# Kernel tuning notes

Hardware: AMD Instinct MI355X
Metric: run time of the kernel (lower is better)

Reference implementation:

```python
import jax, jax.numpy as jnp
import numpy as np


def setup_inputs() -> dict:
    key = jax.random.key(0)
    ks = jax.random.split(key, 8)
    B, T, H, Hu = 128, 64, 1024, 512
    MJW = 64                    # max_jump_width
    J = 2 * MJW + 1             # size_jump_width_set_nn = 129
    N = 2 * T                   # HMM states (word states + null states)
    I = 64                      # source sentence length
    sc = 0.02
    return {
        "y_hidden": jax.random.normal(ks[0], (B, T, H), jnp.float32),
        # emission probs p(source word i | state s), strictly positive for log
        "emission": jax.random.uniform(ks[1], (B, N, I), jnp.float32, 1e-4, 1.0),
        "source_lengths": jax.random.randint(ks[2], (B,), 1, I + 1),
        "W1": jax.random.normal(ks[3], (H, Hu), jnp.float32) * sc,
        "b1": jnp.zeros((Hu,), jnp.float32),
        "W2": jax.random.normal(ks[4], (Hu, J), jnp.float32) * sc,
        "b2": jnp.zeros((J,), jnp.float32),
        "W3": jax.random.normal(ks[5], (Hu, 1), jnp.float32) * sc,
        "b3": jnp.zeros((1,), jnp.float32),
        "max_jump_width": MJW,
    }


def _build_transition(y_hidden, W1, b1, W2, b2, W3, b3, mjw):
    # Dense(tanh) -> Dense softmax jump-width distribution + Dense sigmoid p0
    B, T, _ = y_hidden.shape
    ts = jnp.tanh(y_hidden @ W1 + b1)                       # [B,T,Hu]
    jw = jax.nn.softmax(ts @ W2 + b2, axis=-1)              # [B,T,J]
    p0 = jax.nn.sigmoid(jnp.squeeze(ts @ W3 + b3, -1))      # [B,T]
    r = jnp.arange(T)
    # banded gather: transition[i, j] = jw[i, mjw + j - i]
    band_idx = mjw + r[None, :] - r[:, None]                # [T,T], in [0, J)
    band = jnp.take_along_axis(jw, band_idx[None], axis=2)  # [B,T,T]
    diag_p0 = jnp.eye(T, dtype=jw.dtype) * p0[:, :, None]   # [B,T,T]
    top = jnp.concatenate([band, diag_p0], axis=2)          # [B,T,2T]
    return jnp.concatenate([top, top], axis=1)              # [B,2T,2T]


def _forward_alignment(transition, emission, source_lengths):
    # Faithful translation of the tf.scan forward algorithm. tf.scan with no
    # initializer uses elems[0] as the initial accumulator and emits it as
    # output[0] (log part = ones, so the [0,0] element is 1.0).
    B, N, I = emission.shape
    em = jnp.transpose(emission, (2, 0, 1))                 # [I,B,N]
    alpha0 = jnp.broadcast_to(em[0][:, None, :], (B, N, N)) # rows all equal e_0
    L0 = jnp.ones((B,), emission.dtype)

    def step(carry, e):
        alpha, L = carry                                    # [B,N,N], [B]
        yi = e[:, None, :]                                  # rows of yi_prob identical
        m1 = jnp.matmul(alpha, transition)                  # [B,N,N]
        tmp = m1 * yi
        tmp = tmp / jnp.sum(tmp, axis=2, keepdims=True)     # row-normalized alpha
        m2 = jnp.matmul(transition, alpha) * yi             # [B,N,N]
        max_j = jnp.max(m2, axis=-1)[:, 0]                  # gather row 0 -> [B]
        state_prev = jnp.sum(m1, axis=1)                    # [B,N]
        state = jnp.log(e) + jnp.log(state_prev) - max_j[:, None]
        state_log = jnp.log(jnp.sum(jnp.exp(state), axis=-1))
        L_new = L + state_log + max_j                       # [B]
        return (tmp, L_new), L_new

    (_, _), logs = jax.lax.scan(step, (alpha0, L0), em[1:])  # [I-1,B]
    logs = jnp.concatenate([L0[None], logs], axis=0).T       # [B,I]
    idx = (source_lengths - 1)[:, None]
    return jnp.take_along_axis(logs, idx, axis=1)[:, 0]      # [B]


def reference(y_hidden, emission, source_lengths, W1, b1, W2, b2, W3, b3, max_jump_width):
    transition = _build_transition(y_hidden, W1, b1, W2, b2, W3, b3, max_jump_width)
    return _forward_alignment(transition, emission, source_lengths)
```

## Files before the change

kernel.cpp:

```cpp
#include <hip/hip_runtime.h>
#include <hip/hip_bf16.h>

typedef float f32x4 __attribute__((ext_vector_type(4)));
typedef __bf16 bf16x8 __attribute__((ext_vector_type(8)));
typedef unsigned short u16;

#define OFF_W1T  0u
#define OFF_W23B 1048576u
#define OFF_TS   1196032u

static __device__ __forceinline__ u16 f2bf(float x) {
    __bf16 h = (__bf16)x;
    return __builtin_bit_cast(u16, h);
}

__device__ __forceinline__ void gload16(const void* g, void* l) {
    __builtin_amdgcn_global_load_lds(
        (const __attribute__((address_space(1))) void*)g,
        (__attribute__((address_space(3))) void*)l,
        16, 0, 0);
}

__global__ __launch_bounds__(256) void prep_kernel(
    const float* __restrict__ W1, const float* __restrict__ W2,
    const float* __restrict__ W3,
    __bf16* __restrict__ W1T, __bf16* __restrict__ W23B)
{
    const int t = threadIdx.x;
    if (blockIdx.x < 128) {
        __shared__ __bf16 lds_t[64][72];
        const int kt = blockIdx.x >> 3, nt = blockIdx.x & 7;
        const int k0 = kt * 64, n0 = nt * 64;
        {
            const int kr = t >> 2, c0 = (t & 3) * 16;
            const float* src = W1 + (size_t)(k0 + kr) * 512 + n0 + c0;
            #pragma unroll
            for (int q = 0; q < 4; ++q) {
                float4 v = *(const float4*)(src + q * 4);
                lds_t[kr][c0 + q * 4 + 0] = (__bf16)v.x;
                lds_t[kr][c0 + q * 4 + 1] = (__bf16)v.y;
                lds_t[kr][c0 + q * 4 + 2] = (__bf16)v.z;
                lds_t[kr][c0 + q * 4 + 3] = (__bf16)v.w;
            }
        }
        __syncthreads();
        {
            const int nr = t >> 2, kc = (t & 3) * 16;
            bf16x8 o0, o1;
            #pragma unroll
            for (int j = 0; j < 8; ++j) o0[j] = lds_t[kc + j][nr];
            #pragma unroll
            for (int j = 0; j < 8; ++j) o1[j] = lds_t[kc + 8 + j][nr];
            __bf16* dst = W1T + (size_t)(n0 + nr) * 1024 + k0 + kc;
            *(bf16x8*)(dst)     = o0;
            *(bf16x8*)(dst + 8) = o1;
        }
    } else {
        int g = (blockIdx.x - 128) * 256 + t;
        if (g < 9216) {
            int n = g >> 6;
            int k8 = (g & 63) * 8;
            bf16x8 v;
            #pragma unroll
            for (int j = 0; j < 8; ++j) {
                int k = k8 + j;
                float x = 0.0f;
                if (n < 129) x = W2[(size_t)k * 129 + n];
                else if (n == 129) x = W3[k];
                v[j] = (__bf16)x;
            }
            int kk = k8 >> 5, lg = (k8 >> 3) & 3, ct = n >> 4, lr = n & 15;
            *(bf16x8*)&W23B[(((size_t)(kk * 9 + ct)) * 64 + lg * 16 + lr) * 8] = v;
        }
    }
}

__global__ __launch_bounds__(256, 2) void gemm1_kernel(
    const float* __restrict__ Y, const __bf16* __restrict__ W1T,
    const float* __restrict__ b1, u16* __restrict__ ts)
{
    __shared__ float  As[3][64 * 32];
    __shared__ __bf16 Bs[3][128 * 32];
    const int tid = threadIdx.x;
    const int m0 = blockIdx.x * 64, n0 = blockIdx.y * 128;
    const int wid = tid >> 6, lane = tid & 63;
    const int wr = wid >> 1, wc = wid & 1;
    const int lr = lane & 15, lg = lane >> 4;

    const int al = lane >> 3;
    const int au = (lane & 7) ^ al;
    const float* yA0 = Y + (size_t)(m0 + (wid * 2 + 0) * 8 + al) * 1024 + au * 4;
    const float* yA1 = Y + (size_t)(m0 + (wid * 2 + 1) * 8 + al) * 1024 + au * 4;
    const int bl = lane >> 2;
    const int bu = (lane & 3) ^ (bl & 3);
    const __bf16* wB0 = W1T + (size_t)(n0 + (wid * 2 + 0) * 16 + bl) * 1024 + bu * 8;
    const __bf16* wB1 = W1T + (size_t)(n0 + (wid * 2 + 1) * 16 + bl) * 1024 + bu * 8;

    f32x4 acc[2][4];
    #pragma unroll
    for (int m = 0; m < 2; m++)
        #pragma unroll
        for (int n = 0; n < 4; n++) { f32x4 z = {0.f,0.f,0.f,0.f}; acc[m][n] = z; }

#define STAGE(buf, kt) do { \
    gload16(yA0 + (kt) * 32, &As[buf][(wid * 2 + 0) * 256]); \
    gload16(yA1 + (kt) * 32, &As[buf][(wid * 2 + 1) * 256]); \
    gload16(wB0 + (kt) * 32, &Bs[buf][(wid * 2 + 0) * 512]); \
    gload16(wB1 + (kt) * 32, &Bs[buf][(wid * 2 + 1) * 512]); \
} while (0)

#define COMPUTE(buf) do { \
    bf16x8 af[2]; bf16x8 bfr[4]; \
    _Pragma("unroll") \
    for (int m = 0; m < 2; ++m) { \
        const int row = wr * 32 + m * 16 + lr; \
        const int r7 = row & 7; \
        float4 h0 = *(const float4*)&As[buf][row * 32 + (((lg * 2 + 0) ^ r7) * 4)]; \
        float4 h1 = *(const float4*)&As[buf][row * 32 + (((lg * 2 + 1) ^ r7) * 4)]; \
        bf16x8 tt; \
        tt[0]=(__bf16)h0.x; tt[1]=(__bf16)h0.y; tt[2]=(__bf16)h0.z; tt[3]=(__bf16)h0.w; \
        tt[4]=(__bf16)h1.x; tt[5]=(__bf16)h1.y; tt[6]=(__bf16)h1.z; tt[7]=(__bf16)h1.w; \
        af[m] = tt; \
    } \
    _Pragma("unroll") \
    for (int n = 0; n < 4; ++n) { \
        const int rowb = wc * 64 + n * 16 + lr; \
        bfr[n] = *(const bf16x8*)&Bs[buf][rowb * 32 + ((lg ^ (rowb & 3)) * 8)]; \
    } \
    __builtin_amdgcn_s_setprio(1); \
    _Pragma("unroll") \
    for (int m = 0; m < 2; ++m) \
        _Pragma("unroll") \
        for (int n = 0; n < 4; ++n) \
            acc[m][n] = __builtin_amdgcn_mfma_f32_16x16x32_bf16(af[m], bfr[n], acc[m][n], 0, 0, 0); \
    __builtin_amdgcn_s_setprio(0); \
} while (0)

#define KSTEP(buf, kt, VM, DO_STAGE) do { \
    asm volatile("s_waitcnt vmcnt(" #VM ")" ::: "memory"); \
    __builtin_amdgcn_s_barrier(); \
    COMPUTE(buf); \
    asm volatile("s_waitcnt lgkmcnt(0)" ::: "memory"); \
    __builtin_amdgcn_s_barrier(); \
    if (DO_STAGE) STAGE(buf, (kt) + 3); \
} while (0)

    STAGE(0, 0); STAGE(1, 1); STAGE(2, 2);
    #pragma unroll 1
    for (int base = 0; base < 27; base += 3) {
        KSTEP(0, base + 0, 8, 1);
        KSTEP(1, base + 1, 8, 1);
        KSTEP(2, base + 2, 8, 1);
    }
    KSTEP(0, 27, 8, 1);
    KSTEP(1, 28, 8, 1);
    KSTEP(2, 29, 8, 0);
    KSTEP(0, 30, 4, 0);
    KSTEP(1, 31, 0, 0);

    #pragma unroll
    for (int m = 0; m < 2; m++) {
        #pragma unroll
        for (int n = 0; n < 4; n++) {
            int col = n0 + wc * 64 + n * 16 + lr;
            float bias = b1[col];
            #pragma unroll
            for (int j = 0; j < 4; j++) {
                int row = m0 + wr * 32 + m * 16 + lg * 4 + j;
                float v = tanhf(acc[m][n][j] + bias);
                ts[(size_t)row * 512 + col] = f2bf(v);
            }
        }
    }
#undef STAGE
#undef COMPUTE
#undef KSTEP
}

__global__ __launch_bounds__(256) void gemm2_recur_kernel(
    const u16* __restrict__ ts, const u16* __restrict__ W23B,
    const float* __restrict__ b2, const float* __restrict__ b3,
    const float* __restrict__ em, const int* __restrict__ slen,
    float* __restrict__ out)
{
    __shared__ float jwT_s[64][65];
    __shared__ float em_s[128][65];
    __shared__ float p0_s[64];
    __shared__ float a_bc[64];
    const int b = blockIdx.x;
    const int tid = threadIdx.x;
    const int w = tid >> 6, lane = tid & 63;
    const int lr = lane & 15, lg = lane >> 4;
    const int r0 = b * 64 + w * 16;

    {
        const float4* eg = (const float4*)(em + (size_t)b * 8192);
        #pragma unroll
        for (int q = 0; q < 8; ++q) {
            int i4 = tid + q * 256;
            float4 v = eg[i4];
            int base = i4 * 4; int n = base >> 6; int ii = base & 63;
            em_s[n][ii] = v.x; em_s[n][ii + 1] = v.y; em_s[n][ii + 2] = v.z; em_s[n][ii + 3] = v.w;
        }
    }

    f32x4 acc[9];
    #pragma unroll
    for (int ct = 0; ct < 9; ct++) { f32x4 z = {0.f,0.f,0.f,0.f}; acc[ct] = z; }

    #pragma unroll 4
    for (int kk = 0; kk < 16; ++kk) {
        bf16x8 a = *(const bf16x8*)(ts + (size_t)(r0 + lr) * 512 + kk * 32 + lg * 8);
        #pragma unroll
        for (int ct = 0; ct < 9; ct++) {
            bf16x8 bv = *(const bf16x8*)(W23B + ((size_t)(kk * 9 + ct) * 64 + lane) * 8);
            acc[ct] = __builtin_amdgcn_mfma_f32_16x16x32_bf16(a, bv, acc[ct], 0, 0, 0);
        }
    }

    float b3v = b3[0];
    #pragma unroll
    for (int j = 0; j < 4; j++) {
        int rloc = w * 16 + lg * 4 + j;
        float v[9];
        float mx = -1e30f;
        #pragma unroll
        for (int ct = 0; ct < 9; ct++) {
            int col = ct * 16 + lr;
            if (col < 129) { float x = acc[ct][j] + b2[col]; v[ct] = x; mx = fmaxf(mx, x); }
            else v[ct] = -1e30f;
        }
        #pragma unroll
        for (int o = 1; o < 16; o <<= 1) mx = fmaxf(mx, __shfl_xor(mx, o));
        float sum = 0.f;
        #pragma unroll
        for (int ct = 0; ct < 9; ct++) {
            int col = ct * 16 + lr;
            if (col < 129) { float e = expf(v[ct] - mx); v[ct] = e; sum += e; }
        }
        #pragma unroll
        for (int o = 1; o < 16; o <<= 1) sum += __shfl_xor(sum, o);
        float inv = 1.0f / sum;
        #pragma unroll
        for (int ct = 0; ct < 9; ct++) {
            int col = ct * 16 + lr;
            int cc = col - 64 + rloc;
            if (col < 129 && cc >= 0 && cc < 64)
                jwT_s[cc][rloc] = v[ct] * inv;
        }
        if (lr == 1) {
            float pv = acc[8][j] + b3v;
            p0_s[rloc] = 1.0f / (1.0f + expf(-pv));
        }
    }
    __syncthreads();
    if (tid >= 64) return;

    const int c = tid;
    f32x4 bregv[16];
    #pragma unroll
    for (int q = 0; q < 16; ++q)
        bregv[q] = *(const f32x4*)&jwT_s[c][q * 4];
    const float p0r = p0_s[c];
    const int idx = slen[b] - 1;

    float ut = em_s[c][0] + em_s[c + 64][0];
    float Lacc = 0.f;

    #pragma unroll 1
    for (int i = 1; i <= idx; ++i) {
        a_bc[c] = ut;
        float aloc = ut;
        asm volatile("s_waitcnt lgkmcnt(0)" ::: "memory");
        float s0 = 0.f, s1 = 0.f, s2 = 0.f, s3 = 0.f;
        #pragma unroll
        for (int q = 0; q < 16; ++q) {
            float4 av = *(const float4*)&a_bc[q * 4];
            s0 = fmaf(av.x, bregv[q][0], s0);
            s1 = fmaf(av.y, bregv[q][1], s1);
            s2 = fmaf(av.z, bregv[q][2], s2);
            s3 = fmaf(av.w, bregv[q][3], s3);
        }
        ut = ((s0 + s1) + (s2 + s3)) * em_s[c][i] + aloc * p0r * em_s[c + 64][i];
        if (((i & 3) == 0) || (i == idx)) {
            float r = ut;
            #pragma unroll
            for (int o = 1; o < 64; o <<= 1) r += __shfl_xor(r, o);
            Lacc += __log2f(r);
            ut *= __builtin_amdgcn_rcpf(r);
        }
    }
    if (c == 0) out[b] = 1.0f + 0.6931471805599453f * (Lacc + 7.0f * (float)idx);
}

extern "C" void kernel_launch(void* const* d_in, const int* in_sizes, int n_in,
                              void* d_out, int out_size, void* d_ws, size_t ws_size,
                              hipStream_t stream)
{
    const float* Y   = (const float*)d_in[0];
    const float* em  = (const float*)d_in[1];
    const int*   sl  = (const int*)d_in[2];
    const float* W1  = (const float*)d_in[3];
    const float* b1  = (const float*)d_in[4];
    const float* W2  = (const float*)d_in[5];
    const float* b2  = (const float*)d_in[6];
    const float* W3  = (const float*)d_in[7];
    const float* b3  = (const float*)d_in[8];
    float* out = (float*)d_out;
    char* ws = (char*)d_ws;

    __bf16* W1T  = (__bf16*)(ws + OFF_W1T);
    __bf16* W23B = (__bf16*)(ws + OFF_W23B);
    u16*    ts   = (u16*)(ws + OFF_TS);

    prep_kernel<<<164, 256, 0, stream>>>(W1, W2, W3, W1T, W23B);
    dim3 g1(128, 4);
    gemm1_kernel<<<g1, 256, 0, stream>>>(Y, W1T, b1, ts);
    gemm2_recur_kernel<<<128, 256, 0, stream>>>(ts, (const u16*)W23B, b2, b3, em, sl, out);
}
```

Before: 87.06 us.

## Split band/recurrence kernels, interleave two batches per wave, remap gemm1 blocks

The fused gemm2+recurrence kernel is split in two. A band kernel writes jwT and p0 to workspace, and a 64-thread recurrence kernel runs two batch items per wave. Their LDS clusters are written in inline asm so that one item's math overlaps the other's LDS latency. Per-step normalization is replaced by exponent extraction and power-of-two rescaling, with the log taken only once at the end. gemm1 also gets a 1D XCD-aware block remap, occupancy 3, a different B swizzle, and a single-barrier pipeline loop. The extra launch and global round-trip for jwT/p0 are the cost, and the recurrence now runs on 64 single-wave blocks.

Result: slower. 103.9 us (+19.3%).

```diff
diff --git a/kernel.cpp b/kernel.cpp
--- a/kernel.cpp
+++ b/kernel.cpp
@@ -8,6 +8,8 @@
 #define OFF_W1T  0u
 #define OFF_W23B 1048576u
 #define OFF_TS   1196032u
+#define OFF_JWT  9584640u
+#define OFF_P0   11681792u
 
 static __device__ __forceinline__ u16 f2bf(float x) {
     __bf16 h = (__bf16)x;
@@ -75,24 +77,30 @@
     }
 }
 
-__global__ __launch_bounds__(256, 2) void gemm1_kernel(
+__global__ __launch_bounds__(256, 3) void gemm1_kernel(
     const float* __restrict__ Y, const __bf16* __restrict__ W1T,
     const float* __restrict__ b1, u16* __restrict__ ts)
 {
     __shared__ float  As[3][64 * 32];
     __shared__ __bf16 Bs[3][128 * 32];
     const int tid = threadIdx.x;
-    const int m0 = blockIdx.x * 64, n0 = blockIdx.y * 128;
+    const int bid = blockIdx.x;
+    const int half = bid >> 8;
+    const int b8 = bid & 255;
+    const int xcd = b8 & 7;
+    const int ii = b8 >> 3;
+    const int rb = half * 64 + xcd * 8 + (ii >> 2);
+    const int tb = ii & 3;
+    const int m0 = rb * 64, n0 = tb * 128;
     const int wid = tid >> 6, lane = tid & 63;
     const int wr = wid >> 1, wc = wid & 1;
     const int lr = lane & 15, lg = lane >> 4;
-
     const int al = lane >> 3;
     const int au = (lane & 7) ^ al;
     const float* yA0 = Y + (size_t)(m0 + (wid * 2 + 0) * 8 + al) * 1024 + au * 4;
     const float* yA1 = Y + (size_t)(m0 + (wid * 2 + 1) * 8 + al) * 1024 + au * 4;
     const int bl = lane >> 2;
-    const int bu = (lane & 3) ^ (bl & 3);
+    const int bu = (lane & 3) ^ ((bl >> 1) & 3);
     const __bf16* wB0 = W1T + (size_t)(n0 + (wid * 2 + 0) * 16 + bl) * 1024 + bu * 8;
     const __bf16* wB1 = W1T + (size_t)(n0 + (wid * 2 + 1) * 16 + bl) * 1024 + bu * 8;
 
@@ -125,7 +133,7 @@
     _Pragma("unroll") \
     for (int n = 0; n < 4; ++n) { \
         const int rowb = wc * 64 + n * 16 + lr; \
-        bfr[n] = *(const bf16x8*)&Bs[buf][rowb * 32 + ((lg ^ (rowb & 3)) * 8)]; \
+        bfr[n] = *(const bf16x8*)&Bs[buf][rowb * 32 + ((lg ^ ((rowb >> 1) & 3)) * 8)]; \
     } \
     __builtin_amdgcn_s_setprio(1); \
     _Pragma("unroll") \
@@ -136,27 +144,25 @@
     __builtin_amdgcn_s_setprio(0); \
 } while (0)
 
-#define KSTEP(buf, kt, VM, DO_STAGE) do { \
-    asm volatile("s_waitcnt vmcnt(" #VM ")" ::: "memory"); \
-    __builtin_amdgcn_s_barrier(); \
-    COMPUTE(buf); \
-    asm volatile("s_waitcnt lgkmcnt(0)" ::: "memory"); \
-    __builtin_amdgcn_s_barrier(); \
-    if (DO_STAGE) STAGE(buf, (kt) + 3); \
-} while (0)
-
-    STAGE(0, 0); STAGE(1, 1); STAGE(2, 2);
-    #pragma unroll 1
-    for (int base = 0; base < 27; base += 3) {
-        KSTEP(0, base + 0, 8, 1);
-        KSTEP(1, base + 1, 8, 1);
-        KSTEP(2, base + 2, 8, 1);
-    }
-    KSTEP(0, 27, 8, 1);
-    KSTEP(1, 28, 8, 1);
-    KSTEP(2, 29, 8, 0);
-    KSTEP(0, 30, 4, 0);
-    KSTEP(1, 31, 0, 0);
+    STAGE(0, 0); STAGE(1, 1);
+    {
+        int buf = 0, sbuf = 2;
+        #pragma unroll 1
+        for (int kt = 0; kt < 30; ++kt) {
+            asm volatile("s_waitcnt vmcnt(4)" ::: "memory");
+            __builtin_amdgcn_s_barrier();
+            COMPUTE(buf);
+            STAGE(sbuf, kt + 2);
+            buf  = (buf  == 2) ? 0 : buf  + 1;
+            sbuf = (sbuf == 2) ? 0 : sbuf + 1;
+        }
+    }
+    asm volatile("s_waitcnt vmcnt(4)" ::: "memory");
+    __builtin_amdgcn_s_barrier();
+    COMPUTE(0);
+    asm volatile("s_waitcnt vmcnt(0)" ::: "memory");
+    __builtin_amdgcn_s_barrier();
+    COMPUTE(1);
 
     #pragma unroll
     for (int m = 0; m < 2; m++) {
@@ -174,36 +180,19 @@
     }
 #undef STAGE
 #undef COMPUTE
-#undef KSTEP
-}
-
-__global__ __launch_bounds__(256) void gemm2_recur_kernel(
+}
+
+__global__ __launch_bounds__(256) void band_kernel(
     const u16* __restrict__ ts, const u16* __restrict__ W23B,
     const float* __restrict__ b2, const float* __restrict__ b3,
-    const float* __restrict__ em, const int* __restrict__ slen,
-    float* __restrict__ out)
+    float* __restrict__ jwT, float* __restrict__ p0)
 {
-    __shared__ float jwT_s[64][65];
-    __shared__ float em_s[128][65];
-    __shared__ float p0_s[64];
-    __shared__ float a_bc[64];
     const int b = blockIdx.x;
     const int tid = threadIdx.x;
     const int w = tid >> 6, lane = tid & 63;
     const int lr = lane & 15, lg = lane >> 4;
     const int r0 = b * 64 + w * 16;
 
-    {
-        const float4* eg = (const float4*)(em + (size_t)b * 8192);
-        #pragma unroll
-        for (int q = 0; q < 8; ++q) {
-            int i4 = tid + q * 256;
-            float4 v = eg[i4];
-            int base = i4 * 4; int n = base >> 6; int ii = base & 63;
-            em_s[n][ii] = v.x; em_s[n][ii + 1] = v.y; em_s[n][ii + 2] = v.z; em_s[n][ii + 3] = v.w;
-        }
-    }
-
     f32x4 acc[9];
     #pragma unroll
     for (int ct = 0; ct < 9; ct++) { f32x4 z = {0.f,0.f,0.f,0.f}; acc[ct] = z; }
@@ -246,52 +235,164 @@
             int col = ct * 16 + lr;
             int cc = col - 64 + rloc;
             if (col < 129 && cc >= 0 && cc < 64)
-                jwT_s[cc][rloc] = v[ct] * inv;
+                jwT[((size_t)b * 64 + cc) * 64 + rloc] = v[ct] * inv;
         }
         if (lr == 1) {
             float pv = acc[8][j] + b3v;
-            p0_s[rloc] = 1.0f / (1.0f + expf(-pv));
-        }
-    }
+            p0[b * 64 + rloc] = 1.0f / (1.0f + expf(-pv));
+        }
+    }
+}
+
+#define CLUSTER(OUT, ut, waddr, rbase, emaddr) \
+    asm volatile( \
+        "ds_write_b32 %19, %18\n\t" \
+        "ds_read_b128 %0, %20 offset:0\n\t" \
+        "ds_read_b128 %1, %20 offset:16\n\t" \
+        "ds_read_b128 %2, %20 offset:32\n\t" \
+        "ds_read_b128 %3, %20 offset:48\n\t" \
+        "ds_read_b128 %4, %20 offset:64\n\t" \
+        "ds_read_b128 %5, %20 offset:80\n\t" \
+        "ds_read_b128 %6, %20 offset:96\n\t" \
+        "ds_read_b128 %7, %20 offset:112\n\t" \
+        "ds_read_b128 %8, %20 offset:128\n\t" \
+        "ds_read_b128 %9, %20 offset:144\n\t" \
+        "ds_read_b128 %10, %20 offset:160\n\t" \
+        "ds_read_b128 %11, %20 offset:176\n\t" \
+        "ds_read_b128 %12, %20 offset:192\n\t" \
+        "ds_read_b128 %13, %20 offset:208\n\t" \
+        "ds_read_b128 %14, %20 offset:224\n\t" \
+        "ds_read_b128 %15, %20 offset:240\n\t" \
+        "ds_read_b32 %16, %21\n\t" \
+        "ds_read_b32 %17, %21 offset:256" \
+        : "=&v"(OUT##0), "=&v"(OUT##1), "=&v"(OUT##2),  "=&v"(OUT##3), \
+          "=&v"(OUT##4), "=&v"(OUT##5), "=&v"(OUT##6),  "=&v"(OUT##7), \
+          "=&v"(OUT##8), "=&v"(OUT##9), "=&v"(OUT##10), "=&v"(OUT##11), \
+          "=&v"(OUT##12),"=&v"(OUT##13),"=&v"(OUT##14), "=&v"(OUT##15), \
+          "=&v"(OUT##lo), "=&v"(OUT##hi) \
+        : "v"(ut), "v"(waddr), "v"(rbase), "v"(emaddr) \
+        : "memory")
+
+__global__ __launch_bounds__(64, 1) void recur2_kernel(
+    const float* __restrict__ jwT, const float* __restrict__ p0g,
+    const float* __restrict__ em, const int* __restrict__ slen,
+    float* __restrict__ out)
+{
+    __shared__ float emT[2][63][128];
+    __shared__ f32x4 a_bc[2][16];
+    const int b2 = blockIdx.x, c = threadIdx.x;
+    const int bA = 2 * b2, bB = 2 * b2 + 1;
+
+    const float* bbA = jwT + ((size_t)bA * 64 + c) * 64;
+    const float* bbB = jwT + ((size_t)bB * 64 + c) * 64;
+    f32x4 BA0=*(const f32x4*)(bbA+0),  BA1=*(const f32x4*)(bbA+4),  BA2=*(const f32x4*)(bbA+8),  BA3=*(const f32x4*)(bbA+12);
+    f32x4 BA4=*(const f32x4*)(bbA+16), BA5=*(const f32x4*)(bbA+20), BA6=*(const f32x4*)(bbA+24), BA7=*(const f32x4*)(bbA+28);
+    f32x4 BA8=*(const f32x4*)(bbA+32), BA9=*(const f32x4*)(bbA+36), BA10=*(const f32x4*)(bbA+40),BA11=*(const f32x4*)(bbA+44);
+    f32x4 BA12=*(const f32x4*)(bbA+48),BA13=*(const f32x4*)(bbA+52),BA14=*(const f32x4*)(bbA+56),BA15=*(const f32x4*)(bbA+60);
+    f32x4 BB0=*(const f32x4*)(bbB+0),  BB1=*(const f32x4*)(bbB+4),  BB2=*(const f32x4*)(bbB+8),  BB3=*(const f32x4*)(bbB+12);
+    f32x4 BB4=*(const f32x4*)(bbB+16), BB5=*(const f32x4*)(bbB+20), BB6=*(const f32x4*)(bbB+24), BB7=*(const f32x4*)(bbB+28);
+    f32x4 BB8=*(const f32x4*)(bbB+32), BB9=*(const f32x4*)(bbB+36), BB10=*(const f32x4*)(bbB+40),BB11=*(const f32x4*)(bbB+44);
+    f32x4 BB12=*(const f32x4*)(bbB+48),BB13=*(const f32x4*)(bbB+52),BB14=*(const f32x4*)(bbB+56),BB15=*(const f32x4*)(bbB+60);
+
+    #pragma unroll 1
+    for (int X = 0; X < 2; ++X) {
+        const float4* eg = (const float4*)(em + (size_t)(bA + X) * 8192);
+        #pragma unroll 4
+        for (int q = 0; q < 32; ++q) {
+            int i4 = c + q * 64;
+            float4 v = eg[i4];
+            int n = 4 * q + (c >> 4);
+            int i0 = (c & 15) * 4;
+            #pragma unroll
+            for (int j = 0; j < 4; ++j) {
+                int r = i0 + j;
+                if (r >= 1 && r < 64) emT[X][r - 1][n] = (&v.x)[j];
+            }
+        }
+    }
+    const float p0A = p0g[bA * 64 + c], p0B = p0g[bB * 64 + c];
+    const int idxA = slen[bA] - 1, idxB = slen[bB] - 1;
+    const int maxidx = idxA > idxB ? idxA : idxB;
     __syncthreads();
-    if (tid >= 64) return;
-
-    const int c = tid;
-    f32x4 bregv[16];
-    #pragma unroll
-    for (int q = 0; q < 16; ++q)
-        bregv[q] = *(const f32x4*)&jwT_s[c][q * 4];
-    const float p0r = p0_s[c];
-    const int idx = slen[b] - 1;
-
-    float ut = em_s[c][0] + em_s[c + 64][0];
-    float Lacc = 0.f;
+
+    float utA = em[(size_t)bA * 8192 + c * 64] + em[(size_t)bA * 8192 + (c + 64) * 64];
+    float utB = em[(size_t)bB * 8192 + c * 64] + em[(size_t)bB * 8192 + (c + 64) * 64];
+    int EaccA = 0, EaccB = 0;
+
+    unsigned rbaseA = (unsigned)(uintptr_t)(__attribute__((address_space(3))) void*)&a_bc[0][0];
+    unsigned rbaseB = (unsigned)(uintptr_t)(__attribute__((address_space(3))) void*)&a_bc[1][0];
+    unsigned waA = rbaseA + (unsigned)c * 4u;
+    unsigned waB = rbaseB + (unsigned)c * 4u;
+    unsigned embA = (unsigned)(uintptr_t)(__attribute__((address_space(3))) void*)&emT[0][0][0];
+    unsigned embB = (unsigned)(uintptr_t)(__attribute__((address_space(3))) void*)&emT[1][0][0];
+
+    float emloA = emT[0][0][c], emhiA = emT[0][0][c + 64];
+    float emloB = emT[1][0][c], emhiB = emT[1][0][c + 64];
 
     #pragma unroll 1
-    for (int i = 1; i <= idx; ++i) {
-        a_bc[c] = ut;
-        float aloc = ut;
+    for (int i = 1; i <= maxidx; ++i) {
+        int ei = (i <= 62) ? i : 0;
+        unsigned eaA = embA + (unsigned)(ei * 512 + c * 4);
+        unsigned eaB = embB + (unsigned)(ei * 512 + c * 4);
+        f32x4 A0,A1,A2,A3,A4,A5,A6,A7,A8,A9,A10,A11,A12,A13,A14,A15; float Alo, Ahi;
+        CLUSTER(A, utA, waA, rbaseA, eaA);
+        int bitsA = __builtin_amdgcn_readfirstlane(__float_as_int(utA));
+        int efA = (bitsA >> 23) & 255;
+        EaccA += (i <= idxA) ? (efA - 127) : 0;
+        float scaleA = __int_as_float((254 - efA) << 23);
+        float eAlo = emloA * scaleA, eAhi = emhiA * p0A * scaleA;
+        f32x4 C0,C1,C2,C3,C4,C5,C6,C7,C8,C9,C10,C11,C12,C13,C14,C15; float Clo, Chi;
+        CLUSTER(C, utB, waB, rbaseB, eaB);
+        int bitsB = __builtin_amdgcn_readfirstlane(__float_as_int(utB));
+        int efB = (bitsB >> 23) & 255;
+        EaccB += (i <= idxB) ? (efB - 127) : 0;
+        float scaleB = __int_as_float((254 - efB) << 23);
+        float eBlo = emloB * scaleB, eBhi = emhiB * p0B * scaleB;
+
+        asm volatile("s_waitcnt lgkmcnt(15)" ::: "memory");
+        __builtin_amdgcn_sched_barrier(0);
+        {
+            f32x4 va = A0 * BA0,  vb = A1 * BA1,  vc = A2 * BA2,  vd = A3 * BA3;
+            va = va + A4 * BA4;   vb = vb + A5 * BA5;   vc = vc + A6 * BA6;   vd = vd + A7 * BA7;
+            va = va + A8 * BA8;   vb = vb + A9 * BA9;   vc = vc + A10 * BA10; vd = vd + A11 * BA11;
+            va = va + A12 * BA12; vb = vb + A13 * BA13; vc = vc + A14 * BA14; vd = vd + A15 * BA15;
+            f32x4 vs = (va + vb) + (vc + vd);
+            float sum = (vs[0] + vs[1]) + (vs[2] + vs[3]);
+            float nut = sum * eAlo + utA * eAhi;
+            utA = (i <= idxA) ? nut : utA;
+        }
         asm volatile("s_waitcnt lgkmcnt(0)" ::: "memory");
-        float s0 = 0.f, s1 = 0.f, s2 = 0.f, s3 = 0.f;
-        #pragma unroll
-        for (int q = 0; q < 16; ++q) {
-            float4 av = *(const float4*)&a_bc[q * 4];
-            s0 = fmaf(av.x, bregv[q][0], s0);
-            s1 = fmaf(av.y, bregv[q][1], s1);
-            s2 = fmaf(av.z, bregv[q][2], s2);
-            s3 = fmaf(av.w, bregv[q][3], s3);
-        }
-        ut = ((s0 + s1) + (s2 + s3)) * em_s[c][i] + aloc * p0r * em_s[c + 64][i];
-        if (((i & 3) == 0) || (i == idx)) {
-            float r = ut;
-            #pragma unroll
-            for (int o = 1; o < 64; o <<= 1) r += __shfl_xor(r, o);
-            Lacc += __log2f(r);
-            ut *= __builtin_amdgcn_rcpf(r);
-        }
-    }
-    if (c == 0) out[b] = 1.0f + 0.6931471805599453f * (Lacc + 7.0f * (float)idx);
-}
+        __builtin_amdgcn_sched_barrier(0);
+        {
+            f32x4 va = C0 * BB0,  vb = C1 * BB1,  vc = C2 * BB2,  vd = C3 * BB3;
+            va = va + C4 * BB4;   vb = vb + C5 * BB5;   vc = vc + C6 * BB6;   vd = vd + C7 * BB7;
+            va = va + C8 * BB8;   vb = vb + C9 * BB9;   vc = vc + C10 * BB10; vd = vd + C11 * BB11;
+            va = va + C12 * BB12; vb = vb + C13 * BB13; vc = vc + C14 * BB14; vd = vd + C15 * BB15;
+            f32x4 vs = (va + vb) + (vc + vd);
+            float sum = (vs[0] + vs[1]) + (vs[2] + vs[3]);
+            float nut = sum * eBlo + utB * eBhi;
+            utB = (i <= idxB) ? nut : utB;
+        }
+        emloA = Alo; emhiA = Ahi;
+        emloB = Clo; emhiB = Chi;
+    }
+
+    float rA = utA;
+    #pragma unroll
+    for (int o = 1; o < 64; o <<= 1) rA += __shfl_xor(rA, o);
+    float rB = utB;
+    #pragma unroll
+    for (int o = 1; o < 64; o <<= 1) rB += __shfl_xor(rB, o);
+    if (c == 0) {
+        out[bA] = (idxA > 0)
+            ? 1.0f + 0.6931471805599453f * ((float)EaccA + __log2f(rA) + 7.0f * (float)idxA)
+            : 1.0f;
+        out[bB] = (idxB > 0)
+            ? 1.0f + 0.6931471805599453f * ((float)EaccB + __log2f(rB) + 7.0f * (float)idxB)
+            : 1.0f;
+    }
+}
+#undef CLUSTER
 
 extern "C" void kernel_launch(void* const* d_in, const int* in_sizes, int n_in,
                               void* d_out, int out_size, void* d_ws, size_t ws_size,
@@ -312,9 +413,11 @@
     __bf16* W1T  = (__bf16*)(ws + OFF_W1T);
     __bf16* W23B = (__bf16*)(ws + OFF_W23B);
     u16*    ts   = (u16*)(ws + OFF_TS);
+    float*  jwT  = (float*)(ws + OFF_JWT);
+    float*  p0   = (float*)(ws + OFF_P0);
 
     prep_kernel<<<164, 256, 0, stream>>>(W1, W2, W3, W1T, W23B);
-    dim3 g1(128, 4);
-    gemm1_kernel<<<g1, 256, 0, stream>>>(Y, W1T, b1, ts);
-    gemm2_recur_kernel<<<128, 256, 0, stream>>>(ts, (const u16*)W23B, b2, b3, em, sl, out);
-}
+    gemm1_kernel<<<512, 256, 0, stream>>>(Y, W1T, b1, ts);
+    band_kernel<<<128, 256, 0, stream>>>(ts, (const u16*)W23B, b2, b3, jwT, p0);
+    recur2_kernel<<<64, 64, 0, stream>>>(jwT, p0, em, sl, out);
+}
```
